# Kernel tuning notes

Hardware: AMD Instinct MI355X
Metric: run time of the kernel (lower is better)

The kernel has to match this reference:

```python
import jax, jax.numpy as jnp
import numpy as np

# Qwen2 MoE MLP layer: top-k router -> token dispatch -> grouped SwiGLU MLP -> weighted combine.
S, B, H = 2048, 1, 1024      # seq, batch, hidden
E, K, F = 8, 2, 1408         # num_experts, top_k, moe_intermediate (fc1 emits 2*F for SwiGLU)

def setup_inputs() -> dict:
    key = jax.random.key(0)
    k1, k2, k3, k4 = jax.random.split(key, 4)
    return {
        "hidden_states": jax.random.normal(k1, (S, B, H), jnp.float32),
        "router_weight": jax.random.normal(k2, (H, E), jnp.float32) * 0.02,
        "w1": jax.random.normal(k3, (E, H, 2 * F), jnp.float32) * 0.02,  # grouped fc1 (gate|up)
        "w2": jax.random.normal(k4, (E, F, H), jnp.float32) * 0.02,      # grouped fc2
    }

def reference(hidden_states, router_weight, w1, w2):
    s, b, h = hidden_states.shape
    x = hidden_states.reshape(-1, h)                      # [T, H], T = S*B
    logits = x @ router_weight                            # [T, E]
    probs = jax.nn.softmax(logits, axis=-1)
    _, topk_idx = jax.lax.top_k(probs, K)                 # token -> top-k expert ids
    routing_map = jax.nn.one_hot(topk_idx, E, dtype=probs.dtype).sum(axis=1)  # [T, E] 0/1 mask
    local_probs = probs * routing_map                     # combine weights, zero off-topk
    # Grouped SwiGLU MLP. The torch module permutes tokens to expert groups and runs
    # grouped GEMMs; with static shapes the equivalent math is dense-per-expert with
    # the routing mask folded into the combine weights (identical output).
    y = jnp.einsum('th,ehf->tef', x, w1)                  # [T, E, 2F]
    y1, y2 = jnp.split(y, 2, axis=-1)
    g = jax.nn.silu(y1) * y2                              # swiglu, [T, E, F]
    o = jnp.einsum('tef,efh->teh', g, w2)                 # [T, E, H]
    out = jnp.einsum('teh,te->th', o, local_probs)        # unpermute + prob-weighted combine
    return out.reshape(s, b, h)
```

## Files before the change

### kernel.cpp

```cpp
#include <hip/hip_runtime.h>
#include <hip/hip_bf16.h>
#include <stdint.h>

#define T_TOK 2048
#define HD    1024
#define NE    8
#define FD    1408
#define F2D   2816
#define HP    1056
#define OP    1056

#define BM 128
#define BK 32
#define MAXMT 40
#define MAXSLOTS 5120
#define FC1_NT 22
#define FC2_NT 16
#define FC1_NWG (FC1_NT * MAXMT)
#define FC2_NWG (FC2_NT * MAXMT)
#define FC1_CHUNK 110
#define FC2_CHUNK 80

#define PREP_TR1 2816
#define PREP_TR2 1408
#define PREP_ROUTER 512
#define PREP_NWG (PREP_TR1 + PREP_TR2 + PREP_ROUTER)

typedef __attribute__((ext_vector_type(8))) short bf16x8;
typedef __attribute__((ext_vector_type(4))) float f32x4;

__device__ __forceinline__ unsigned short f2bf(float f) {
  unsigned int u = __float_as_uint(f);
  u += 0x7FFFu + ((u >> 16) & 1u);
  return (unsigned short)(u >> 16);
}

#define GLL16(gp, lp) __builtin_amdgcn_global_load_lds( \
    (const __attribute__((address_space(1))) void*)(gp), \
    (__attribute__((address_space(3))) void*)(lp), 16, 0, 0)

__global__ __launch_bounds__(256) void k_prep(
    const float* __restrict__ x,  const float* __restrict__ rw,
    const float* __restrict__ w1, const float* __restrict__ w2,
    unsigned short* __restrict__ w1t, unsigned short* __restrict__ w2t,
    unsigned short* __restrict__ xbf, int* __restrict__ ctrl,
    int* __restrict__ tok_e, float* __restrict__ tok_p)
{
  const int b = blockIdx.x;
  if (b < PREP_TR1 + PREP_TR2) {
    const float* src; unsigned short* dst; int C, DP, r0, c0;
    if (b < PREP_TR1) {
      const int z = b / 352, rem = b % 352;
      C = F2D; DP = HP;
      r0 = (rem / 44) * 128; c0 = (rem % 44) * 64;
      src = w1 + (size_t)z * HD * F2D;
      dst = w1t + (size_t)z * F2D * HP;
    } else {
      const int bb = b - PREP_TR1;
      const int z = bb / 176, rem = bb % 176;
      C = HD; DP = FD;
      r0 = (rem / 16) * 128; c0 = (rem % 16) * 64;
      src = w2 + (size_t)z * FD * HD;
      dst = w2t + (size_t)z * HD * FD;
    }
    __shared__ float tile[128 * 65];
    const int t = threadIdx.x;
#pragma unroll
    for (int i = 0; i < 8; ++i) {
      const int q = i * 256 + t;
      const int row = q >> 4, c4 = q & 15;
      float4 v = *reinterpret_cast<const float4*>(
          &src[(size_t)(r0 + row) * C + c0 + c4 * 4]);
      float* d = &tile[row * 65 + c4 * 4];
      d[0] = v.x; d[1] = v.y; d[2] = v.z; d[3] = v.w;
    }
    __syncthreads();
#pragma unroll
    for (int i = 0; i < 4; ++i) {
      const int p = i * 256 + t;
      const int c = p >> 4, seg = p & 15;
      unsigned short u[8];
#pragma unroll
      for (int j = 0; j < 8; ++j) u[j] = f2bf(tile[(seg * 8 + j) * 65 + c]);
      *reinterpret_cast<uint4*>(&dst[(size_t)(c0 + c) * DP + r0 + seg * 8]) =
          *reinterpret_cast<const uint4*>(u);
    }
    return;
  }

  const int lane = threadIdx.x & 63;
  const int t = (b - PREP_TR1 - PREP_TR2) * 4 + (threadIdx.x >> 6);
  const float* xr = x + (size_t)t * HD;

  float part[8];
#pragma unroll
  for (int e = 0; e < 8; ++e) part[e] = 0.f;

#pragma unroll
  for (int i = 0; i < 16; ++i) {
    const int h = i * 64 + lane;
    const float xv = xr[h];
    xbf[(size_t)t * HP + h] = f2bf(xv);
    const float4* rwr = reinterpret_cast<const float4*>(rw + (size_t)h * 8);
    float4 a = rwr[0], bb = rwr[1];
    part[0] += xv * a.x; part[1] += xv * a.y; part[2] += xv * a.z; part[3] += xv * a.w;
    part[4] += xv * bb.x; part[5] += xv * bb.y; part[6] += xv * bb.z; part[7] += xv * bb.w;
  }
#pragma unroll
  for (int e = 0; e < 8; ++e) {
    float v = part[e];
#pragma unroll
    for (int d = 32; d; d >>= 1) v += __shfl_xor(v, d, 64);
    part[e] = v;
  }
  float m = part[0];
#pragma unroll
  for (int e = 1; e < 8; ++e) m = fmaxf(m, part[e]);
  float p[8], s = 0.f;
#pragma unroll
  for (int e = 0; e < 8; ++e) { p[e] = __expf(part[e] - m); s += p[e]; }
  const float inv = 1.f / s;
#pragma unroll
  for (int e = 0; e < 8; ++e) p[e] *= inv;

  int e0 = 0; float p0 = p[0];
#pragma unroll
  for (int e = 1; e < 8; ++e) if (p[e] > p0) { p0 = p[e]; e0 = e; }
  int e1 = -1; float p1 = -1.f;
#pragma unroll
  for (int e = 0; e < 8; ++e) if (e != e0 && p[e] > p1) { p1 = p[e]; e1 = e; }

  if (lane == 0) {
    tok_e[t * 2 + 0] = e0; tok_e[t * 2 + 1] = e1;
    tok_p[t * 2 + 0] = p0; tok_p[t * 2 + 1] = p1;
    atomicAdd(&ctrl[e0], 1);
    atomicAdd(&ctrl[e1], 1);
  }
}

__global__ __launch_bounds__(256) void k_offsets(
    int* __restrict__ ctrl, int* __restrict__ stok, float* __restrict__ sp,
    int* __restrict__ widmt1, int* __restrict__ widmt2)
{
  __shared__ int soff[8], scnt[8], sFirst[8], sNmt[8], sTake[8];
  __shared__ int sSpill;
  if (threadIdx.x == 0) {
    int o = 0, nm = 0, spill = 0;
    for (int e = 0; e < 8; ++e) {
      ctrl[16 + e] = o; soff[e] = o; scnt[e] = ctrl[e];
      const int n = ctrl[e];
      const int nmt = (n + BM - 1) / BM;
      sFirst[e] = nm; sNmt[e] = nmt; sTake[e] = nmt < 5 ? nmt : 5;
      if (nmt > 5) spill = 1;
      for (int j = 0; j < nmt; ++j) { ctrl[24 + nm] = e; ctrl[64 + nm] = o + j * BM; ++nm; }
      o += nmt * BM;
    }
    for (int i = nm; i < MAXMT; ++i) ctrl[24 + i] = -1;
    sSpill = spill;
  }
  __syncthreads();
  for (int i = threadIdx.x; i < FC1_NWG; i += 256) {
    const int e = i / FC1_CHUNK, r = i % FC1_CHUNK;
    const int j = r / FC1_NT, n = r % FC1_NT;
    widmt1[i] = (j < sTake[e]) ? (sFirst[e] + j) * 32 + n : -1;
  }
  for (int i = threadIdx.x; i < FC2_NWG; i += 256) {
    const int e = i / FC2_CHUNK, r = i % FC2_CHUNK;
    const int j = r / FC2_NT, n = r % FC2_NT;
    widmt2[i] = (j < sTake[e]) ? (sFirst[e] + j) * 32 + n : -1;
  }
  __syncthreads();
  if (sSpill && threadIdx.x == 0) {
    int cur = 0;
    for (int e = 0; e < 8; ++e)
      for (int j = 5; j < sNmt[e]; ++j)
        for (int n = 0; n < FC1_NT; ++n) {
          while (widmt1[cur] != -1) ++cur;
          widmt1[cur] = (sFirst[e] + j) * 32 + n;
        }
    cur = 0;
    for (int e = 0; e < 8; ++e)
      for (int j = 5; j < sNmt[e]; ++j)
        for (int n = 0; n < FC2_NT; ++n) {
          while (widmt2[cur] != -1) ++cur;
          widmt2[cur] = (sFirst[e] + j) * 32 + n;
        }
  }
  for (int e = 0; e < 8; ++e) {
    const int n = scnt[e], o = soff[e];
    const int padEnd = (n + BM - 1) / BM * BM;
    for (int j = n + (int)threadIdx.x; j < padEnd; j += 256) {
      stok[o + j] = 0; sp[o + j] = 0.f;
    }
  }
}

__global__ __launch_bounds__(256) void k_scatter(
    int* __restrict__ ctrl, const int* __restrict__ tok_e,
    const float* __restrict__ tok_p, int* __restrict__ stok,
    float* __restrict__ sp, int* __restrict__ tslot)
{
  const int t = blockIdx.x * 256 + threadIdx.x;
#pragma unroll
  for (int k = 0; k < 2; ++k) {
    const int e = tok_e[t * 2 + k];
    const float pp = tok_p[t * 2 + k];
    const int pos = atomicAdd(&ctrl[8 + e], 1);
    const int slot = ctrl[16 + e] + pos;
    stok[slot] = t; sp[slot] = pp;
    tslot[t * 2 + k] = slot;
  }
}

__global__ __launch_bounds__(256) void k_fc1(
    const unsigned short* __restrict__ xbf,
    const unsigned short* __restrict__ w1t,
    const int* __restrict__ ctrl,
    const int* __restrict__ stok,
    const float* __restrict__ sp,
    const int* __restrict__ widmt1,
    unsigned short* __restrict__ g)
{
  const int bid = blockIdx.x;
  const int wid = (bid & 7) * FC1_CHUNK + (bid >> 3);
  const int packed = widmt1[wid];
  if (packed < 0) return;
  const int mt = packed >> 5;
  const int e = ctrl[24 + mt];
  const int rowbase = ctrl[64 + mt];
  const int n0 = (packed & 31) * 64;

  __shared__ unsigned short sA[3][BM * BK];
  __shared__ unsigned short sB1[3][64 * BK];
  __shared__ unsigned short sB2[3][64 * BK];

  const int tid = threadIdx.x;
  const int lane = tid & 63;
  const int wave = tid >> 6;
  const int wm = wave >> 1, wn = wave & 1;

  const int schunk = (lane & 3) ^ ((lane >> 3) & 3);
  const unsigned short* aSrc[2];
#pragma unroll
  for (int t4 = 0; t4 < 2; ++t4) {
    const int row = (t4 * 4 + wave) * 16 + (lane >> 2);
    const int tok = stok[rowbase + row];
    aSrc[t4] = xbf + (size_t)tok * HP + schunk * 8;
  }
  const int brow = wave * 16 + (lane >> 2);
  const unsigned short* b1Src = w1t + (size_t)(e * F2D + n0 + brow) * HP + schunk * 8;
  const unsigned short* b2Src = w1t + (size_t)(e * F2D + FD + n0 + brow) * HP + schunk * 8;

  const int c = lane >> 4;
  int aoff[4], boff[2];
#pragma unroll
  for (int m = 0; m < 4; ++m) {
    const int row = wm * 64 + m * 16 + (lane & 15);
    aoff[m] = row * 32 + ((c ^ ((row >> 1) & 3)) << 3);
  }
#pragma unroll
  for (int n = 0; n < 2; ++n) {
    const int row = wn * 32 + n * 16 + (lane & 15);
    boff[n] = row * 32 + ((c ^ ((row >> 1) & 3)) << 3);
  }

  const f32x4 zero = {0.f, 0.f, 0.f, 0.f};
  f32x4 acc1[4][2], acc2[4][2];
#pragma unroll
  for (int m = 0; m < 4; ++m)
#pragma unroll
    for (int n = 0; n < 2; ++n) { acc1[m][n] = zero; acc2[m][n] = zero; }

  auto STAGE = [&](int buf, int k0) {
#pragma unroll
    for (int t4 = 0; t4 < 2; ++t4)
      GLL16(aSrc[t4] + k0, &sA[buf][(t4 * 4 + wave) * 512]);
    GLL16(b1Src + k0, &sB1[buf][wave * 512]);
    GLL16(b2Src + k0, &sB2[buf][wave * 512]);
  };

  const int NSTEP = HD / BK;
  STAGE(0, 0);
  STAGE(1, BK);
  int bsel = 0;
  for (int t = 0; t < NSTEP; ++t) {
    if (t < NSTEP - 2) { asm volatile("s_waitcnt vmcnt(4)" ::: "memory"); }
    else               { asm volatile("s_waitcnt vmcnt(0)" ::: "memory"); }
    __builtin_amdgcn_s_barrier();
    __builtin_amdgcn_sched_barrier(0);
    if (t + 2 < NSTEP) {
      int bnext = bsel + 2; if (bnext >= 3) bnext -= 3;
      STAGE(bnext, (t + 2) * BK);
    }
    bf16x8 af[4], b1f[2], b2f[2];
#pragma unroll
    for (int m = 0; m < 4; ++m)
      af[m] = *(const bf16x8*)&sA[bsel][aoff[m]];
#pragma unroll
    for (int n = 0; n < 2; ++n) {
      b1f[n] = *(const bf16x8*)&sB1[bsel][boff[n]];
      b2f[n] = *(const bf16x8*)&sB2[bsel][boff[n]];
    }
    asm volatile("s_waitcnt lgkmcnt(0)" ::: "memory");
    __builtin_amdgcn_sched_barrier(0);
    __builtin_amdgcn_s_setprio(1);
#pragma unroll
    for (int m = 0; m < 4; ++m)
#pragma unroll
      for (int n = 0; n < 2; ++n) {
        acc1[m][n] = __builtin_amdgcn_mfma_f32_16x16x32_bf16(af[m], b1f[n], acc1[m][n], 0, 0, 0);
        acc2[m][n] = __builtin_amdgcn_mfma_f32_16x16x32_bf16(af[m], b2f[n], acc2[m][n], 0, 0, 0);
      }
    __builtin_amdgcn_s_setprio(0);
    bsel = bsel + 1 == 3 ? 0 : bsel + 1;
  }

  float prv[4][4];
#pragma unroll
  for (int m = 0; m < 4; ++m)
#pragma unroll
    for (int r = 0; r < 4; ++r)
      prv[m][r] = sp[rowbase + wm * 64 + m * 16 + (lane >> 4) * 4 + r];

#pragma unroll
  for (int m = 0; m < 4; ++m) {
    const int rb = rowbase + wm * 64 + m * 16 + (lane >> 4) * 4;
#pragma unroll
    for (int n = 0; n < 2; ++n) {
      const int col = n0 + wn * 32 + n * 16 + (lane & 15);
#pragma unroll
      for (int r = 0; r < 4; ++r) {
        const float y1 = acc1[m][n][r];
        const float y2 = acc2[m][n][r];
        const float gv = y1 / (1.f + __expf(-y1)) * y2 * prv[m][r];
        g[(size_t)(rb + r) * FD + col] = f2bf(gv);
      }
    }
  }
}

__global__ __launch_bounds__(256) void k_fc2(
    const unsigned short* __restrict__ g,
    const unsigned short* __restrict__ w2t,
    const int* __restrict__ ctrl,
    const int* __restrict__ widmt2,
    float* __restrict__ o)
{
  const int bid = blockIdx.x;
  const int wid = (bid & 7) * FC2_CHUNK + (bid >> 3);
  const int packed = widmt2[wid];
  if (packed < 0) return;
  const int mt = packed >> 5;
  const int e = ctrl[24 + mt];
  const int rowbase = ctrl[64 + mt];
  const int n0 = (packed & 31) * 64;

  __shared__ unsigned short sA[3][BM * BK];
  __shared__ unsigned short sB[3][64 * BK];

  const int tid = threadIdx.x;
  const int lane = tid & 63;
  const int wave = tid >> 6;
  const int wm = wave >> 1, wn = wave & 1;

  const int schunk = (lane & 3) ^ ((lane >> 3) & 3);
  const unsigned short* aSrc[2];
#pragma unroll
  for (int t4 = 0; t4 < 2; ++t4) {
    const int row = (t4 * 4 + wave) * 16 + (lane >> 2);
    aSrc[t4] = g + (size_t)(rowbase + row) * FD + schunk * 8;
  }
  const int brow = wave * 16 + (lane >> 2);
  const unsigned short* bSrc = w2t + (size_t)(e * HD + n0 + brow) * FD + schunk * 8;

  const int c = lane >> 4;
  int aoff[4], boff[2];
#pragma unroll
  for (int m = 0; m < 4; ++m) {
    const int row = wm * 64 + m * 16 + (lane & 15);
    aoff[m] = row * 32 + ((c ^ ((row >> 1) & 3)) << 3);
  }
#pragma unroll
  for (int n = 0; n < 2; ++n) {
    const int row = wn * 32 + n * 16 + (lane & 15);
    boff[n] = row * 32 + ((c ^ ((row >> 1) & 3)) << 3);
  }

  const f32x4 zero = {0.f, 0.f, 0.f, 0.f};
  f32x4 acc[4][2];
#pragma unroll
  for (int m = 0; m < 4; ++m)
#pragma unroll
    for (int n = 0; n < 2; ++n) acc[m][n] = zero;

  auto STAGE = [&](int buf, int k0) {
#pragma unroll
    for (int t4 = 0; t4 < 2; ++t4)
      GLL16(aSrc[t4] + k0, &sA[buf][(t4 * 4 + wave) * 512]);
    GLL16(bSrc + k0, &sB[buf][wave * 512]);
  };

  const int NSTEP = FD / BK;
  STAGE(0, 0);
  STAGE(1, BK);
  int bsel = 0;
  for (int t = 0; t < NSTEP; ++t) {
    if (t < NSTEP - 2) { asm volatile("s_waitcnt vmcnt(3)" ::: "memory"); }
    else               { asm volatile("s_waitcnt vmcnt(0)" ::: "memory"); }
    __builtin_amdgcn_s_barrier();
    __builtin_amdgcn_sched_barrier(0);
    if (t + 2 < NSTEP) {
      int bnext = bsel + 2; if (bnext >= 3) bnext -= 3;
      STAGE(bnext, (t + 2) * BK);
    }
    bf16x8 af[4], bf[2];
#pragma unroll
    for (int m = 0; m < 4; ++m)
      af[m] = *(const bf16x8*)&sA[bsel][aoff[m]];
#pragma unroll
    for (int n = 0; n < 2; ++n)
      bf[n] = *(const bf16x8*)&sB[bsel][boff[n]];
    asm volatile("s_waitcnt lgkmcnt(0)" ::: "memory");
    __builtin_amdgcn_sched_barrier(0);
    __builtin_amdgcn_s_setprio(1);
#pragma unroll
    for (int m = 0; m < 4; ++m)
#pragma unroll
      for (int n = 0; n < 2; ++n)
        acc[m][n] = __builtin_amdgcn_mfma_f32_16x16x32_bf16(af[m], bf[n], acc[m][n], 0, 0, 0);
    __builtin_amdgcn_s_setprio(0);
    bsel = bsel + 1 == 3 ? 0 : bsel + 1;
  }

#pragma unroll
  for (int m = 0; m < 4; ++m) {
    const int rb = rowbase + wm * 64 + m * 16 + (lane >> 4) * 4;
#pragma unroll
    for (int n = 0; n < 2; ++n) {
      const int col = n0 + wn * 32 + n * 16 + (lane & 15);
#pragma unroll
      for (int r = 0; r < 4; ++r)
        o[(size_t)(rb + r) * OP + col] = acc[m][n][r];
    }
  }
}

__global__ __launch_bounds__(256) void k_combine(
    const float* __restrict__ o, const int* __restrict__ tslot,
    float* __restrict__ out)
{
  const int t = blockIdx.x;
  const int c4 = threadIdx.x;
  const int sA = tslot[t * 2], sB = tslot[t * 2 + 1];
  const float4 a = reinterpret_cast<const float4*>(o + (size_t)sA * OP)[c4];
  const float4 b = reinterpret_cast<const float4*>(o + (size_t)sB * OP)[c4];
  float4 r;
  r.x = a.x + b.x; r.y = a.y + b.y; r.z = a.z + b.z; r.w = a.w + b.w;
  reinterpret_cast<float4*>(out)[(size_t)t * 256 + c4] = r;
}

extern "C" void kernel_launch(void* const* d_in, const int* in_sizes, int n_in,
                              void* d_out, int out_size, void* d_ws, size_t ws_size,
                              hipStream_t stream)
{
  const float* x  = (const float*)d_in[0];
  const float* rw = (const float*)d_in[1];
  const float* w1 = (const float*)d_in[2];
  const float* w2 = (const float*)d_in[3];
  float* out = (float*)d_out;
  char* ws = (char*)d_ws;

  int*   ctrl   = (int*)(ws + 0);
  int*   tok_e  = (int*)(ws + 1024);
  float* tok_p  = (float*)(ws + 17408);
  int*   stok   = (int*)(ws + 33792);
  float* sp     = (float*)(ws + 54272);
  int*   tslot  = (int*)(ws + 74752);
  int*   widmt1 = (int*)(ws + 91136);
  int*   widmt2 = (int*)(ws + 94656);
  unsigned short* xbf = (unsigned short*)(ws + 97280);
  unsigned short* w1t = (unsigned short*)(ws + 4422656);
  unsigned short* w2t = (unsigned short*)(ws + 52001792);
  unsigned short* g   = (unsigned short*)(ws + 75070464);
  float* o = (float*)(ws + 4422656);

  hipMemsetAsync(ws, 0, 1024, stream);

  k_prep<<<PREP_NWG, 256, 0, stream>>>(x, rw, w1, w2, w1t, w2t, xbf, ctrl, tok_e, tok_p);
  k_offsets<<<1, 256, 0, stream>>>(ctrl, stok, sp, widmt1, widmt2);
  k_scatter<<<T_TOK / 256, 256, 0, stream>>>(ctrl, tok_e, tok_p, stok, sp, tslot);
  k_fc1<<<FC1_NWG, 256, 0, stream>>>(xbf, w1t, ctrl, stok, sp, widmt1, g);
  k_fc2<<<FC2_NWG, 256, 0, stream>>>(g, w2t, ctrl, widmt2, o);
  k_combine<<<T_TOK, 256, 0, stream>>>(o, tslot, out);
}
```

Before: 205.5 us.

## Drop weight transpose in prep; use LDS transpose reads for B operands

The prep kernel now converts w1 and w2 to bf16 in their original row-major [K,N] layout with a plain streaming cast, instead of running an LDS-tiled transpose. The fc1 and fc2 GEMMs stage B tiles K-major and use ds_read_b64_tr_b16 to transpose them on the fly into MFMA operand fragments. This removes the strided transpose writes and shared-memory round trip from the prep pass, which handles large weight tensors. In exchange, the GEMM B loads now stride by a full row per k, and the LDS layout has no swizzle, so bank conflicts are possible.

```diff
diff --git a/kernel.cpp b/kernel.cpp
--- a/kernel.cpp
+++ b/kernel.cpp
@@ -8,6 +8,7 @@
 #define FD    1408
 #define F2D   2816
 #define HP    1056
+#define W2P   1056
 #define OP    1056
 
 #define BM 128
@@ -21,13 +22,14 @@
 #define FC1_CHUNK 110
 #define FC2_CHUNK 80
 
-#define PREP_TR1 2816
-#define PREP_TR2 1408
+#define PREP_W1 5632
+#define PREP_W2 2816
 #define PREP_ROUTER 512
-#define PREP_NWG (PREP_TR1 + PREP_TR2 + PREP_ROUTER)
+#define PREP_NWG (PREP_W1 + PREP_W2 + PREP_ROUTER)
 
 typedef __attribute__((ext_vector_type(8))) short bf16x8;
 typedef __attribute__((ext_vector_type(4))) float f32x4;
+typedef __attribute__((ext_vector_type(2))) int i32x2;
 
 __device__ __forceinline__ unsigned short f2bf(float f) {
   unsigned int u = __float_as_uint(f);
@@ -39,57 +41,61 @@
     (const __attribute__((address_space(1))) void*)(gp), \
     (__attribute__((address_space(3))) void*)(lp), 16, 0, 0)
 
+#define LDS_OFF(p) ((unsigned)(uintptr_t)(__attribute__((address_space(3))) const unsigned short*)(p))
+
+__device__ __forceinline__ void tr_issue(unsigned a, i32x2& lo, i32x2& hi) {
+  asm volatile("ds_read_b64_tr_b16 %0, %2\n\t"
+               "ds_read_b64_tr_b16 %1, %2 offset:512"
+               : "=&v"(lo), "=&v"(hi)
+               : "v"(a)
+               : "memory");
+}
+__device__ __forceinline__ bf16x8 tr_pack(i32x2 lo, i32x2 hi) {
+  union { i32x2 v; short s[4]; } a, b;
+  a.v = lo; b.v = hi;
+  bf16x8 f;
+  f[0] = a.s[0]; f[1] = a.s[1]; f[2] = a.s[2]; f[3] = a.s[3];
+  f[4] = b.s[0]; f[5] = b.s[1]; f[6] = b.s[2]; f[7] = b.s[3];
+  return f;
+}
+
 __global__ __launch_bounds__(256) void k_prep(
     const float* __restrict__ x,  const float* __restrict__ rw,
     const float* __restrict__ w1, const float* __restrict__ w2,
-    unsigned short* __restrict__ w1t, unsigned short* __restrict__ w2t,
+    unsigned short* __restrict__ w1bf, unsigned short* __restrict__ w2bf,
     unsigned short* __restrict__ xbf, int* __restrict__ ctrl,
     int* __restrict__ tok_e, float* __restrict__ tok_p)
 {
   const int b = blockIdx.x;
-  if (b < PREP_TR1 + PREP_TR2) {
-    const float* src; unsigned short* dst; int C, DP, r0, c0;
-    if (b < PREP_TR1) {
-      const int z = b / 352, rem = b % 352;
-      C = F2D; DP = HP;
-      r0 = (rem / 44) * 128; c0 = (rem % 44) * 64;
-      src = w1 + (size_t)z * HD * F2D;
-      dst = w1t + (size_t)z * F2D * HP;
-    } else {
-      const int bb = b - PREP_TR1;
-      const int z = bb / 176, rem = bb % 176;
-      C = HD; DP = FD;
-      r0 = (rem / 16) * 128; c0 = (rem % 16) * 64;
-      src = w2 + (size_t)z * FD * HD;
-      dst = w2t + (size_t)z * HD * FD;
-    }
-    __shared__ float tile[128 * 65];
-    const int t = threadIdx.x;
-#pragma unroll
-    for (int i = 0; i < 8; ++i) {
-      const int q = i * 256 + t;
-      const int row = q >> 4, c4 = q & 15;
-      float4 v = *reinterpret_cast<const float4*>(
-          &src[(size_t)(r0 + row) * C + c0 + c4 * 4]);
-      float* d = &tile[row * 65 + c4 * 4];
-      d[0] = v.x; d[1] = v.y; d[2] = v.z; d[3] = v.w;
-    }
-    __syncthreads();
+  if (b < PREP_W1) {
+    const size_t base4 = (size_t)b * 1024 + threadIdx.x;
 #pragma unroll
     for (int i = 0; i < 4; ++i) {
-      const int p = i * 256 + t;
-      const int c = p >> 4, seg = p & 15;
-      unsigned short u[8];
-#pragma unroll
-      for (int j = 0; j < 8; ++j) u[j] = f2bf(tile[(seg * 8 + j) * 65 + c]);
-      *reinterpret_cast<uint4*>(&dst[(size_t)(c0 + c) * DP + r0 + seg * 8]) =
-          *reinterpret_cast<const uint4*>(u);
+      const size_t idx4 = base4 + i * 256;
+      float4 v = reinterpret_cast<const float4*>(w1)[idx4];
+      ushort4 u;
+      u.x = f2bf(v.x); u.y = f2bf(v.y); u.z = f2bf(v.z); u.w = f2bf(v.w);
+      reinterpret_cast<ushort4*>(w1bf)[idx4] = u;
     }
     return;
   }
+  if (b < PREP_W1 + PREP_W2) {
+    const int bb = b - PREP_W1;
+#pragma unroll
+    for (int i = 0; i < 4; ++i) {
+      const int idx = i * 256 + threadIdx.x;
+      const int row = bb * 4 + (idx >> 8);
+      const int c4 = idx & 255;
+      float4 v = *reinterpret_cast<const float4*>(&w2[(size_t)row * HD + c4 * 4]);
+      ushort4 u;
+      u.x = f2bf(v.x); u.y = f2bf(v.y); u.z = f2bf(v.z); u.w = f2bf(v.w);
+      *reinterpret_cast<ushort4*>(&w2bf[(size_t)row * W2P + c4 * 4]) = u;
+    }
+    return;
+  }
 
   const int lane = threadIdx.x & 63;
-  const int t = (b - PREP_TR1 - PREP_TR2) * 4 + (threadIdx.x >> 6);
+  const int t = (b - PREP_W1 - PREP_W2) * 4 + (threadIdx.x >> 6);
   const float* xr = x + (size_t)t * HD;
 
   float part[8];
@@ -214,7 +220,7 @@
 
 __global__ __launch_bounds__(256) void k_fc1(
     const unsigned short* __restrict__ xbf,
-    const unsigned short* __restrict__ w1t,
+    const unsigned short* __restrict__ w1bf,
     const int* __restrict__ ctrl,
     const int* __restrict__ stok,
     const float* __restrict__ sp,
@@ -247,22 +253,25 @@
     const int tok = stok[rowbase + row];
     aSrc[t4] = xbf + (size_t)tok * HP + schunk * 8;
   }
-  const int brow = wave * 16 + (lane >> 2);
-  const unsigned short* b1Src = w1t + (size_t)(e * F2D + n0 + brow) * HP + schunk * 8;
-  const unsigned short* b2Src = w1t + (size_t)(e * F2D + FD + n0 + brow) * HP + schunk * 8;
+
+  const int kdec = wave * 8 + ((lane >> 5) << 2) + ((lane >> 1) & 3);
+  const int ndec = ((lane >> 3) & 3) * 16 + (lane & 1) * 8;
+  const unsigned short* b1Src = w1bf + ((size_t)e * HD + kdec) * F2D + n0 + ndec;
+  const unsigned short* b2Src = b1Src + FD;
 
   const int c = lane >> 4;
-  int aoff[4], boff[2];
+  int aoff[4];
 #pragma unroll
   for (int m = 0; m < 4; ++m) {
     const int row = wm * 64 + m * 16 + (lane & 15);
     aoff[m] = row * 32 + ((c ^ ((row >> 1) & 3)) << 3);
   }
-#pragma unroll
-  for (int n = 0; n < 2; ++n) {
-    const int row = wn * 32 + n * 16 + (lane & 15);
-    boff[n] = row * 32 + ((c ^ ((row >> 1) & 3)) << 3);
-  }
+  const unsigned trlane = (lane & 15) * 8 + (lane >> 4) * 1024;
+  unsigned trb[2];
+#pragma unroll
+  for (int n = 0; n < 2; ++n) trb[n] = trlane + (wn * 2 + n) * 128;
+  const unsigned b1base = LDS_OFF(&sB1[0][0]);
+  const unsigned b2base = LDS_OFF(&sB2[0][0]);
 
   const f32x4 zero = {0.f, 0.f, 0.f, 0.f};
   f32x4 acc1[4][2], acc2[4][2];
@@ -271,17 +280,19 @@
 #pragma unroll
     for (int n = 0; n < 2; ++n) { acc1[m][n] = zero; acc2[m][n] = zero; }
 
-  auto STAGE = [&](int buf, int k0) {
+  auto STAGE = [&](int buf, int kt) {
+    const size_t kadd = (size_t)kt * BK;
 #pragma unroll
     for (int t4 = 0; t4 < 2; ++t4)
-      GLL16(aSrc[t4] + k0, &sA[buf][(t4 * 4 + wave) * 512]);
-    GLL16(b1Src + k0, &sB1[buf][wave * 512]);
-    GLL16(b2Src + k0, &sB2[buf][wave * 512]);
+      GLL16(aSrc[t4] + kadd, &sA[buf][(t4 * 4 + wave) * 512]);
+    const size_t bkadd = (size_t)kt * BK * F2D;
+    GLL16(b1Src + bkadd, &sB1[buf][wave * 512]);
+    GLL16(b2Src + bkadd, &sB2[buf][wave * 512]);
   };
 
   const int NSTEP = HD / BK;
   STAGE(0, 0);
-  STAGE(1, BK);
+  STAGE(1, 1);
   int bsel = 0;
   for (int t = 0; t < NSTEP; ++t) {
     if (t < NSTEP - 2) { asm volatile("s_waitcnt vmcnt(4)" ::: "memory"); }
@@ -290,19 +301,26 @@
     __builtin_amdgcn_sched_barrier(0);
     if (t + 2 < NSTEP) {
       int bnext = bsel + 2; if (bnext >= 3) bnext -= 3;
-      STAGE(bnext, (t + 2) * BK);
-    }
-    bf16x8 af[4], b1f[2], b2f[2];
+      STAGE(bnext, t + 2);
+    }
+    bf16x8 af[4];
 #pragma unroll
     for (int m = 0; m < 4; ++m)
       af[m] = *(const bf16x8*)&sA[bsel][aoff[m]];
+    i32x2 q1lo[2], q1hi[2], q2lo[2], q2hi[2];
 #pragma unroll
     for (int n = 0; n < 2; ++n) {
-      b1f[n] = *(const bf16x8*)&sB1[bsel][boff[n]];
-      b2f[n] = *(const bf16x8*)&sB2[bsel][boff[n]];
+      tr_issue(b1base + bsel * 4096 + trb[n], q1lo[n], q1hi[n]);
+      tr_issue(b2base + bsel * 4096 + trb[n], q2lo[n], q2hi[n]);
     }
     asm volatile("s_waitcnt lgkmcnt(0)" ::: "memory");
     __builtin_amdgcn_sched_barrier(0);
+    bf16x8 b1f[2], b2f[2];
+#pragma unroll
+    for (int n = 0; n < 2; ++n) {
+      b1f[n] = tr_pack(q1lo[n], q1hi[n]);
+      b2f[n] = tr_pack(q2lo[n], q2hi[n]);
+    }
     __builtin_amdgcn_s_setprio(1);
 #pragma unroll
     for (int m = 0; m < 4; ++m)
@@ -341,7 +359,7 @@
 
 __global__ __launch_bounds__(256) void k_fc2(
     const unsigned short* __restrict__ g,
-    const unsigned short* __restrict__ w2t,
+    const unsigned short* __restrict__ w2bf,
     const int* __restrict__ ctrl,
     const int* __restrict__ widmt2,
     float* __restrict__ o)
@@ -370,21 +388,23 @@
     const int row = (t4 * 4 + wave) * 16 + (lane >> 2);
     aSrc[t4] = g + (size_t)(rowbase + row) * FD + schunk * 8;
   }
-  const int brow = wave * 16 + (lane >> 2);
-  const unsigned short* bSrc = w2t + (size_t)(e * HD + n0 + brow) * FD + schunk * 8;
+
+  const int kdec = wave * 8 + ((lane >> 5) << 2) + ((lane >> 1) & 3);
+  const int ndec = ((lane >> 3) & 3) * 16 + (lane & 1) * 8;
+  const unsigned short* bSrc = w2bf + ((size_t)e * FD + kdec) * W2P + n0 + ndec;
 
   const int c = lane >> 4;
-  int aoff[4], boff[2];
+  int aoff[4];
 #pragma unroll
   for (int m = 0; m < 4; ++m) {
     const int row = wm * 64 + m * 16 + (lane & 15);
     aoff[m] = row * 32 + ((c ^ ((row >> 1) & 3)) << 3);
   }
-#pragma unroll
-  for (int n = 0; n < 2; ++n) {
-    const int row = wn * 32 + n * 16 + (lane & 15);
-    boff[n] = row * 32 + ((c ^ ((row >> 1) & 3)) << 3);
-  }
+  const unsigned trlane = (lane & 15) * 8 + (lane >> 4) * 1024;
+  unsigned trb[2];
+#pragma unroll
+  for (int n = 0; n < 2; ++n) trb[n] = trlane + (wn * 2 + n) * 128;
+  const unsigned bbase = LDS_OFF(&sB[0][0]);
 
   const f32x4 zero = {0.f, 0.f, 0.f, 0.f};
   f32x4 acc[4][2];
@@ -393,16 +413,18 @@
 #pragma unroll
     for (int n = 0; n < 2; ++n) acc[m][n] = zero;
 
-  auto STAGE = [&](int buf, int k0) {
+  auto STAGE = [&](int buf, int kt) {
+    const size_t kadd = (size_t)kt * BK;
 #pragma unroll
     for (int t4 = 0; t4 < 2; ++t4)
-      GLL16(aSrc[t4] + k0, &sA[buf][(t4 * 4 + wave) * 512]);
-    GLL16(bSrc + k0, &sB[buf][wave * 512]);
+      GLL16(aSrc[t4] + kadd, &sA[buf][(t4 * 4 + wave) * 512]);
+    const size_t bkadd = (size_t)kt * BK * W2P;
+    GLL16(bSrc + bkadd, &sB[buf][wave * 512]);
   };
 
   const int NSTEP = FD / BK;
   STAGE(0, 0);
-  STAGE(1, BK);
+  STAGE(1, 1);
   int bsel = 0;
   for (int t = 0; t < NSTEP; ++t) {
     if (t < NSTEP - 2) { asm volatile("s_waitcnt vmcnt(3)" ::: "memory"); }
@@ -411,17 +433,22 @@
     __builtin_amdgcn_sched_barrier(0);
     if (t + 2 < NSTEP) {
       int bnext = bsel + 2; if (bnext >= 3) bnext -= 3;
-      STAGE(bnext, (t + 2) * BK);
-    }
-    bf16x8 af[4], bf[2];
+      STAGE(bnext, t + 2);
+    }
+    bf16x8 af[4];
 #pragma unroll
     for (int m = 0; m < 4; ++m)
       af[m] = *(const bf16x8*)&sA[bsel][aoff[m]];
+    i32x2 qlo[2], qhi[2];
 #pragma unroll
     for (int n = 0; n < 2; ++n)
-      bf[n] = *(const bf16x8*)&sB[bsel][boff[n]];
+      tr_issue(bbase + bsel * 4096 + trb[n], qlo[n], qhi[n]);
     asm volatile("s_waitcnt lgkmcnt(0)" ::: "memory");
     __builtin_amdgcn_sched_barrier(0);
+    bf16x8 bf[2];
+#pragma unroll
+    for (int n = 0; n < 2; ++n)
+      bf[n] = tr_pack(qlo[n], qhi[n]);
     __builtin_amdgcn_s_setprio(1);
 #pragma unroll
     for (int m = 0; m < 4; ++m)
@@ -478,18 +505,18 @@
   int*   tslot  = (int*)(ws + 74752);
   int*   widmt1 = (int*)(ws + 91136);
   int*   widmt2 = (int*)(ws + 94656);
-  unsigned short* xbf = (unsigned short*)(ws + 97280);
-  unsigned short* w1t = (unsigned short*)(ws + 4422656);
-  unsigned short* w2t = (unsigned short*)(ws + 52001792);
-  unsigned short* g   = (unsigned short*)(ws + 75070464);
+  unsigned short* xbf  = (unsigned short*)(ws + 97280);
+  unsigned short* w1bf = (unsigned short*)(ws + 4422656);
+  unsigned short* w2bf = (unsigned short*)(ws + 50560000);
+  unsigned short* g    = (unsigned short*)(ws + 74349568);
   float* o = (float*)(ws + 4422656);
 
   hipMemsetAsync(ws, 0, 1024, stream);
 
-  k_prep<<<PREP_NWG, 256, 0, stream>>>(x, rw, w1, w2, w1t, w2t, xbf, ctrl, tok_e, tok_p);
+  k_prep<<<PREP_NWG, 256, 0, stream>>>(x, rw, w1, w2, w1bf, w2bf, xbf, ctrl, tok_e, tok_p);
   k_offsets<<<1, 256, 0, stream>>>(ctrl, stok, sp, widmt1, widmt2);
   k_scatter<<<T_TOK / 256, 256, 0, stream>>>(ctrl, tok_e, tok_p, stok, sp, tslot);
-  k_fc1<<<FC1_NWG, 256, 0, stream>>>(xbf, w1t, ctrl, stok, sp, widmt1, g);
-  k_fc2<<<FC2_NWG, 256, 0, stream>>>(g, w2t, ctrl, widmt2, o);
+  k_fc1<<<FC1_NWG, 256, 0, stream>>>(xbf, w1bf, ctrl, stok, sp, widmt1, g);
+  k_fc2<<<FC2_NWG, 256, 0, stream>>>(g, w2bf, ctrl, widmt2, o);
   k_combine<<<T_TOK, 256, 0, stream>>>(o, tslot, out);
 }
```

After: 207.8 us. About the same (+1.1%).
